# Performance work log

Measured on AMD Instinct MI355X. Metric: run time of the kernel, lower is better.

Reference implementation:

```python
import jax, jax.numpy as jnp
import numpy as np

B, T, D, H, V = 4096, 30, 512, 1024, 128  # words, MAX_WORD_LEN, input_dim, hidden, num_of_chars

def setup_inputs() -> dict:
    key = jax.random.key(0)
    ks = jax.random.split(key, 8)
    x = jax.random.randint(ks[0], (B, T), 0, V)
    emb = jax.random.normal(ks[1], (V, D), jnp.float32)
    s = 1.0 / np.sqrt(H)  # torch LSTMCell default init range
    W_ih = jax.random.uniform(ks[2], (4 * H, D), jnp.float32, -s, s)
    W_hh = jax.random.uniform(ks[3], (4 * H, H), jnp.float32, -s, s)
    b_ih = jax.random.uniform(ks[4], (4 * H,), jnp.float32, -s, s)
    b_hh = jax.random.uniform(ks[5], (4 * H,), jnp.float32, -s, s)
    xav = np.sqrt(2.0 / (B + H))  # xavier_normal_ std for [B,H] state tensors
    h0 = jax.random.normal(ks[6], (B, H), jnp.float32) * xav
    c0 = jax.random.normal(ks[7], (B, H), jnp.float32) * xav
    return {"x": x, "emb": emb, "W_ih": W_ih, "W_hh": W_hh,
            "b_ih": b_ih, "b_hh": b_hh, "h0": h0, "c0": c0}

def reference(x, emb, W_ih, W_hh, b_ih, b_hh, h0, c0):
    xe = emb[x]                       # [B, T, D] char embeddings
    xs = jnp.swapaxes(xe, 0, 1)       # [T, B, D] for scan over time

    def step(carry, xt):
        h, c = carry
        # torch LSTMCell gate order: i, f, g, o
        gates = xt @ W_ih.T + b_ih + h @ W_hh.T + b_hh  # [B, 4H]
        i, f, g, o = jnp.split(gates, 4, axis=-1)
        c = jax.nn.sigmoid(f) * c + jax.nn.sigmoid(i) * jnp.tanh(g)
        h = jax.nn.sigmoid(o) * jnp.tanh(c)
        return (h, c), None

    (h, c), _ = jax.lax.scan(step, (h0, c0), xs)
    return h
```

## Files before the change

kernel.cpp:

```cpp
#include <hip/hip_runtime.h>
#include <hip/hip_bf16.h>

#define BW    4096
#define TT    30
#define DIN   512
#define HD    1024
#define VCH   128
#define G4    4096

typedef __attribute__((ext_vector_type(8))) __bf16 bf16x8;
typedef __attribute__((ext_vector_type(4))) float  f32x4;

__device__ __forceinline__ ushort f2bf(float f) {
    unsigned u = __float_as_uint(f);
    unsigned r = (u + 0x7fffu + ((u >> 16) & 1u)) >> 16;
    return (ushort)r;
}
__device__ __forceinline__ float sigf(float x) { return 1.f / (1.f + __expf(-x)); }
__device__ __forceinline__ float tanhfast(float x) { return 2.f / (1.f + __expf(-2.f * x)) - 1.f; }


__global__ __launch_bounds__(256) void cvt_bf16_kernel(const float* __restrict__ in,
                                                       ushort* __restrict__ out, int n4) {
    int i = blockIdx.x * 256 + threadIdx.x;
    if (i >= n4) return;
    float4 v = ((const float4*)in)[i];
    ushort4 o;
    o.x = f2bf(v.x); o.y = f2bf(v.y); o.z = f2bf(v.z); o.w = f2bf(v.w);
    ((ushort4*)out)[i] = o;
}

__global__ __launch_bounds__(256) void init_hc_kernel(const float* __restrict__ h0,
                                                      const float* __restrict__ c0,
                                                      ushort* __restrict__ hb,
                                                      float* __restrict__ c, int n4) {
    int i = blockIdx.x * 256 + threadIdx.x;
    if (i >= n4) return;
    float4 v = ((const float4*)h0)[i];
    ushort4 o;
    o.x = f2bf(v.x); o.y = f2bf(v.y); o.z = f2bf(v.z); o.w = f2bf(v.w);
    ((ushort4*)hb)[i] = o;
    ((float4*)c)[i] = ((const float4*)c0)[i];
}

__global__ __launch_bounds__(256) void proj_emb_kernel(const float* __restrict__ emb,
                                                       const float* __restrict__ W_ih,
                                                       const float* __restrict__ b_ih,
                                                       const float* __restrict__ b_hh,
                                                       float* __restrict__ pe) {
    __shared__ float se[8][DIN];
    const int j  = blockIdx.x * 256 + threadIdx.x;
    const int c0 = blockIdx.y * 8;
    for (int i = threadIdx.x; i < 8 * DIN; i += 256)
        se[i >> 9][i & (DIN - 1)] = emb[(size_t)c0 * DIN + i];
    __syncthreads();
    const float* wv = W_ih + (size_t)j * DIN;
    float s[8];
#pragma unroll
    for (int cc = 0; cc < 8; ++cc) s[cc] = 0.f;
    for (int k = 0; k < DIN; k += 4) {
        float4 w4 = *(const float4*)&wv[k];
#pragma unroll
        for (int cc = 0; cc < 8; ++cc)
            s[cc] += se[cc][k] * w4.x + se[cc][k+1] * w4.y + se[cc][k+2] * w4.z + se[cc][k+3] * w4.w;
    }
    const float bias = b_ih[j] + b_hh[j];
    const int g = j >> 10, h = j & 1023;
#pragma unroll
    for (int cc = 0; cc < 8; ++cc)
        pe[(((size_t)(c0 + cc) * HD + h) << 2) + g] = s[cc] + bias;
}


#define STAGE2(AB, SB, SH, SKT)                                                        \
  {                                                                                    \
    ushort* dst0 = &tiles[((((SB)*2 + (AB))*2 + (SH)) * 8192) + (w*2+0)*512];          \
    ushort* dst1 = dst0 + 512;                                                         \
    const ushort *s0, *s1;                                                             \
    if ((AB) == 0) {                                                                   \
      s0 = A + aOff0 + (size_t)(SH)*131072 + (size_t)(SKT)*64;                         \
      s1 = A + aOff1 + (size_t)(SH)*131072 + (size_t)(SKT)*64;                         \
    } else {                                                                           \
      s0 = Bt + bOff[SH][0] + (size_t)(SKT)*64;                                        \
      s1 = Bt + bOff[SH][1] + (size_t)(SKT)*64;                                        \
    }                                                                                  \
    __builtin_amdgcn_global_load_lds((const __attribute__((address_space(1))) void*)s0,\
        (__attribute__((address_space(3))) void*)dst0, 16, 0, 0);                      \
    __builtin_amdgcn_global_load_lds((const __attribute__((address_space(1))) void*)s1,\
        (__attribute__((address_space(3))) void*)dst1, 16, 0, 0);                      \
  }

#define PHASE(BUF, Q, AB, SB, SH, SKT, VM)                                             \
  {                                                                                    \
    const ushort* aT = &tiles[(((BUF)*2 + 0)*2 + haA) * 8192];                         \
    const ushort* bT = &tiles[(((BUF)*2 + 1)*2 + haB) * 8192];                         \
    if ((Q) == 0) {                                                                    \
      _Pragma("unroll")                                                                \
      for (int n = 0; n < 4; ++n) {                                                    \
        bfr[n][0] = *(const bf16x8*)(bT + hbOff + n*1024 + aoff0);                     \
        bfr[n][1] = *(const bf16x8*)(bT + hbOff + n*1024 + aoff1);                     \
      }                                                                                \
    }                                                                                  \
    bf16x8 a00 = *(const bf16x8*)(aT + (2*(Q)+0)*1024 + aoff0);                        \
    bf16x8 a01 = *(const bf16x8*)(aT + (2*(Q)+0)*1024 + aoff1);                        \
    bf16x8 a10 = *(const bf16x8*)(aT + (2*(Q)+1)*1024 + aoff0);                        \
    bf16x8 a11 = *(const bf16x8*)(aT + (2*(Q)+1)*1024 + aoff1);                        \
    STAGE2(AB, SB, SH, SKT);                                                           \
    __builtin_amdgcn_s_barrier();                                                      \
    asm volatile("s_waitcnt lgkmcnt(0)" ::: "memory");                                 \
    __builtin_amdgcn_s_setprio(1);                                                     \
    _Pragma("unroll")                                                                  \
    for (int n = 0; n < 4; ++n) {                                                      \
      acc[2*(Q)+0][n] = __builtin_amdgcn_mfma_f32_16x16x32_bf16(a00, bfr[n][0], acc[2*(Q)+0][n], 0, 0, 0); \
      acc[2*(Q)+0][n] = __builtin_amdgcn_mfma_f32_16x16x32_bf16(a01, bfr[n][1], acc[2*(Q)+0][n], 0, 0, 0); \
      acc[2*(Q)+1][n] = __builtin_amdgcn_mfma_f32_16x16x32_bf16(a10, bfr[n][0], acc[2*(Q)+1][n], 0, 0, 0); \
      acc[2*(Q)+1][n] = __builtin_amdgcn_mfma_f32_16x16x32_bf16(a11, bfr[n][1], acc[2*(Q)+1][n], 0, 0, 0); \
    }                                                                                  \
    __builtin_amdgcn_s_setprio(0);                                                     \
    if (VM) asm volatile("s_waitcnt vmcnt(4)" ::: "memory");                           \
    __builtin_amdgcn_s_barrier();                                                      \
    asm volatile("" ::: "memory");                                                     \
  }

__global__ __launch_bounds__(512, 2) void gemm_cell_kernel(const ushort* __restrict__ A,
                                                           const ushort* __restrict__ Bt,
                                                           const float* __restrict__ peAll,
                                                           const int* __restrict__ x,
                                                           int t, int last,
                                                           float* __restrict__ c,
                                                           ushort* __restrict__ hbN,
                                                           float* __restrict__ hout) {
    __shared__ ushort tiles[65536];

    const int orig = blockIdx.x;
    const int wgid = (orig & 7) * 32 + (orig >> 3);
    const int bm = wgid >> 4, bn = wgid & 15;

    const int tid = threadIdx.x;
    const int w = tid >> 6, l = tid & 63;
    const int fr = l & 15, hi = l >> 4;
    const int haA = w >> 2;
    const int haB = (w >> 1) & 1;
    const int hbOff = (w & 1) * 4096;

    const int r0 = (w * 2 + 0) * 8 + (l >> 3), r1 = r0 + 8;
    const int csrc = (l & 7) ^ (l >> 3);
    const size_t aOff0 = (size_t)(bm * 256 + r0) * 1024 + csrc * 8;
    const size_t aOff1 = (size_t)(bm * 256 + r1) * 1024 + csrc * 8;
    size_t bOff[2][2];
#pragma unroll
    for (int half = 0; half < 2; ++half) {
        const int ra = half * 128 + r0, rb = half * 128 + r1;
        const int na = ((ra >> 4) & 3) * 1024 + bn * 64 + ((ra >> 6) << 4) + (ra & 15);
        const int nb = ((rb >> 4) & 3) * 1024 + bn * 64 + ((rb >> 6) << 4) + (rb & 15);
        bOff[half][0] = (size_t)na * 1024 + csrc * 8;
        bOff[half][1] = (size_t)nb * 1024 + csrc * 8;
    }

    const int aoff0 = fr * 64 + ((hi) ^ (fr & 7)) * 8;
    const int aoff1 = fr * 64 + ((4 + hi) ^ (fr & 7)) * 8;

    f32x4 acc[8][4];
#pragma unroll
    for (int m = 0; m < 8; ++m)
#pragma unroll
        for (int n = 0; n < 4; ++n) acc[m][n] = 0.f;
    bf16x8 bfr[4][2];

    STAGE2(0, 0, 0, 0);
    STAGE2(0, 0, 1, 0);
    STAGE2(1, 0, 0, 0);
    STAGE2(1, 0, 1, 0);
    STAGE2(1, 1, 0, 1);
    STAGE2(1, 1, 1, 1);
    asm volatile("s_waitcnt vmcnt(4)" ::: "memory");
    __builtin_amdgcn_s_barrier();
    asm volatile("" ::: "memory");

    for (int i = 0; i < 8; ++i) {
        const int k0 = 2 * i;
        PHASE(0, 0, 0, 1, 0, k0 + 1, 0);
        PHASE(0, 1, 0, 1, 1, k0 + 1, 0);
        PHASE(0, 2, 1, 0, 0, (k0 + 2) & 15, 0);
        PHASE(0, 3, 1, 0, 1, (k0 + 2) & 15, 1);
        PHASE(1, 0, 0, 0, 0, (k0 + 2) & 15, 0);
        PHASE(1, 1, 0, 0, 1, (k0 + 2) & 15, 0);
        PHASE(1, 2, 1, 1, 0, (k0 + 3) & 15, 0);
        PHASE(1, 3, 1, 1, 1, (k0 + 3) & 15, 1);
    }

    const int h_idx = bn * 64 + (w & 3) * 16 + fr;
    const int bbase = bm * 256 + (w >> 2) * 128 + (hi << 2);
    const float4* pe4 = (const float4*)peAll;
#pragma unroll
    for (int m = 0; m < 8; ++m) {
#pragma unroll
        for (int r = 0; r < 4; ++r) {
            const int b = bbase + m * 16 + r;
            const int ch = x[b * TT + t];
            const float4 pv = pe4[(size_t)ch * HD + h_idx];
            float I = sigf(acc[m][0][r] + pv.x);
            float F = sigf(acc[m][1][r] + pv.y);
            float G = tanhfast(acc[m][2][r] + pv.z);
            float O = sigf(acc[m][3][r] + pv.w);
            const size_t off = (size_t)b * HD + h_idx;
            const float cn = F * c[off] + I * G;
            const float hn = O * tanhfast(cn);
            c[off] = cn;
            hbN[off] = f2bf(hn);
            if (last) hout[off] = hn;
        }
    }
}

extern "C" void kernel_launch(void* const* d_in, const int* in_sizes, int n_in,
                              void* d_out, int out_size, void* d_ws, size_t ws_size,
                              hipStream_t stream) {
    const int*   x    = (const int*)d_in[0];
    const float* emb  = (const float*)d_in[1];
    const float* W_ih = (const float*)d_in[2];
    const float* W_hh = (const float*)d_in[3];
    const float* b_ih = (const float*)d_in[4];
    const float* b_hh = (const float*)d_in[5];
    const float* h0   = (const float*)d_in[6];
    const float* c0   = (const float*)d_in[7];
    float* out = (float*)d_out;

    char* ws = (char*)d_ws;
    ushort* whh = (ushort*)ws;
    float*  pe  = (float*)(ws + (size_t)8388608);
    ushort* hb0 = (ushort*)(ws + (size_t)(8388608 + 2097152));
    ushort* hb1 = (ushort*)(ws + (size_t)(8388608 + 2097152 + 8388608));
    float*  cbuf = (float*)(ws + (size_t)(8388608 + 2097152 + 8388608 + 8388608));

    cvt_bf16_kernel<<<4096, 256, 0, stream>>>(W_hh, whh, (G4 * HD) / 4);
    proj_emb_kernel<<<dim3(16, 16), 256, 0, stream>>>(emb, W_ih, b_ih, b_hh, pe);
    init_hc_kernel<<<4096, 256, 0, stream>>>(h0, c0, hb0, cbuf, (BW * HD) / 4);

    ushort* hbuf[2] = {hb0, hb1};
    for (int t = 0; t < TT; ++t) {
        gemm_cell_kernel<<<256, 512, 0, stream>>>(
            hbuf[t & 1], whh, pe, x, t, (t == TT - 1) ? 1 : 0,
            cbuf, hbuf[(t & 1) ^ 1], out);
    }
}
```

Baseline: 1.628 ms.

## Triple-buffer A tiles in LDS to deepen the GEMM prefetch pipeline

Grows the LDS tile buffer from 128KB to 160KB so that A tiles rotate through three buffers while B keeps two. Global-to-LDS loads for the next K-step can then be issued further ahead, and the vmcnt wait threshold rises from 4 to 8, letting more loads stay in flight behind the MFMA work. The cost is more LDS per block, which may limit blocks per CU, plus runtime-rotated buffer offsets in place of compile-time constants.

```diff
diff --git a/kernel.cpp b/kernel.cpp
--- a/kernel.cpp
+++ b/kernel.cpp
@@ -72,54 +72,54 @@
 }
 
 
-#define STAGE2(AB, SB, SH, SKT)                                                        \
-  {                                                                                    \
-    ushort* dst0 = &tiles[((((SB)*2 + (AB))*2 + (SH)) * 8192) + (w*2+0)*512];          \
-    ushort* dst1 = dst0 + 512;                                                         \
-    const ushort *s0, *s1;                                                             \
-    if ((AB) == 0) {                                                                   \
-      s0 = A + aOff0 + (size_t)(SH)*131072 + (size_t)(SKT)*64;                         \
-      s1 = A + aOff1 + (size_t)(SH)*131072 + (size_t)(SKT)*64;                         \
-    } else {                                                                           \
-      s0 = Bt + bOff[SH][0] + (size_t)(SKT)*64;                                        \
-      s1 = Bt + bOff[SH][1] + (size_t)(SKT)*64;                                        \
-    }                                                                                  \
-    __builtin_amdgcn_global_load_lds((const __attribute__((address_space(1))) void*)s0,\
-        (__attribute__((address_space(3))) void*)dst0, 16, 0, 0);                      \
-    __builtin_amdgcn_global_load_lds((const __attribute__((address_space(1))) void*)s1,\
-        (__attribute__((address_space(3))) void*)dst1, 16, 0, 0);                      \
+#define GLDS(SRC, DST)                                                                  \
+    __builtin_amdgcn_global_load_lds((const __attribute__((address_space(1))) void*)(SRC), \
+        (__attribute__((address_space(3))) void*)(DST), 16, 0, 0)
+
+#define STAGE_A(DSTOFF, SH, KOFF)                                                       \
+  {                                                                                     \
+    ushort* dst0 = &tiles[(DSTOFF) + (SH) * 8192 + w * 1024];                           \
+    GLDS(A + aOff0 + (size_t)(SH) * 131072 + (KOFF), dst0);                             \
+    GLDS(A + aOff1 + (size_t)(SH) * 131072 + (KOFF), dst0 + 512);                       \
   }
 
-#define PHASE(BUF, Q, AB, SB, SH, SKT, VM)                                             \
-  {                                                                                    \
-    const ushort* aT = &tiles[(((BUF)*2 + 0)*2 + haA) * 8192];                         \
-    const ushort* bT = &tiles[(((BUF)*2 + 1)*2 + haB) * 8192];                         \
-    if ((Q) == 0) {                                                                    \
-      _Pragma("unroll")                                                                \
-      for (int n = 0; n < 4; ++n) {                                                    \
-        bfr[n][0] = *(const bf16x8*)(bT + hbOff + n*1024 + aoff0);                     \
-        bfr[n][1] = *(const bf16x8*)(bT + hbOff + n*1024 + aoff1);                     \
-      }                                                                                \
-    }                                                                                  \
-    bf16x8 a00 = *(const bf16x8*)(aT + (2*(Q)+0)*1024 + aoff0);                        \
-    bf16x8 a01 = *(const bf16x8*)(aT + (2*(Q)+0)*1024 + aoff1);                        \
-    bf16x8 a10 = *(const bf16x8*)(aT + (2*(Q)+1)*1024 + aoff0);                        \
-    bf16x8 a11 = *(const bf16x8*)(aT + (2*(Q)+1)*1024 + aoff1);                        \
-    STAGE2(AB, SB, SH, SKT);                                                           \
-    __builtin_amdgcn_s_barrier();                                                      \
-    asm volatile("s_waitcnt lgkmcnt(0)" ::: "memory");                                 \
-    __builtin_amdgcn_s_setprio(1);                                                     \
-    _Pragma("unroll")                                                                  \
-    for (int n = 0; n < 4; ++n) {                                                      \
+#define STAGE_B(BIDX, SH, KOFF)                                                         \
+  {                                                                                     \
+    ushort* dst0 = &tiles[49152 + (BIDX) * 16384 + (SH) * 8192 + w * 1024];             \
+    GLDS(Bt + bOff[SH][0] + (KOFF), dst0);                                              \
+    GLDS(Bt + bOff[SH][1] + (KOFF), dst0 + 512);                                        \
+  }
+
+#define PHASE(ABASE, BIDX, Q, STAGE_STMT, VM)                                           \
+  {                                                                                     \
+    const ushort* aT = &tiles[(ABASE) + haA * 8192];                                    \
+    const ushort* bT = &tiles[49152 + (BIDX) * 16384 + haB * 8192];                     \
+    if ((Q) == 0) {                                                                     \
+      _Pragma("unroll")                                                                 \
+      for (int n = 0; n < 4; ++n) {                                                     \
+        bfr[n][0] = *(const bf16x8*)(bT + hbOff + n * 1024 + aoff0);                    \
+        bfr[n][1] = *(const bf16x8*)(bT + hbOff + n * 1024 + aoff1);                    \
+      }                                                                                 \
+    }                                                                                   \
+    bf16x8 a00 = *(const bf16x8*)(aT + (2 * (Q) + 0) * 1024 + aoff0);                   \
+    bf16x8 a01 = *(const bf16x8*)(aT + (2 * (Q) + 0) * 1024 + aoff1);                   \
+    bf16x8 a10 = *(const bf16x8*)(aT + (2 * (Q) + 1) * 1024 + aoff0);                   \
+    bf16x8 a11 = *(const bf16x8*)(aT + (2 * (Q) + 1) * 1024 + aoff1);                   \
+    STAGE_STMT;                                                                         \
+    __builtin_amdgcn_s_barrier();                                                       \
+    asm volatile("s_waitcnt lgkmcnt(0)" ::: "memory");                                  \
+    __builtin_amdgcn_s_setprio(1);                                                      \
+    _Pragma("unroll")                                                                   \
+    for (int n = 0; n < 4; ++n) {                                                       \
       acc[2*(Q)+0][n] = __builtin_amdgcn_mfma_f32_16x16x32_bf16(a00, bfr[n][0], acc[2*(Q)+0][n], 0, 0, 0); \
       acc[2*(Q)+0][n] = __builtin_amdgcn_mfma_f32_16x16x32_bf16(a01, bfr[n][1], acc[2*(Q)+0][n], 0, 0, 0); \
       acc[2*(Q)+1][n] = __builtin_amdgcn_mfma_f32_16x16x32_bf16(a10, bfr[n][0], acc[2*(Q)+1][n], 0, 0, 0); \
       acc[2*(Q)+1][n] = __builtin_amdgcn_mfma_f32_16x16x32_bf16(a11, bfr[n][1], acc[2*(Q)+1][n], 0, 0, 0); \
-    }                                                                                  \
-    __builtin_amdgcn_s_setprio(0);                                                     \
-    if (VM) asm volatile("s_waitcnt vmcnt(4)" ::: "memory");                           \
-    __builtin_amdgcn_s_barrier();                                                      \
-    asm volatile("" ::: "memory");                                                     \
+    }                                                                                   \
+    __builtin_amdgcn_s_setprio(0);                                                      \
+    if (VM) asm volatile("s_waitcnt vmcnt(8)" ::: "memory");                            \
+    __builtin_amdgcn_s_barrier();                                                       \
+    asm volatile("" ::: "memory");                                                      \
   }
 
 __global__ __launch_bounds__(512, 2) void gemm_cell_kernel(const ushort* __restrict__ A,
@@ -130,7 +130,7 @@
                                                            float* __restrict__ c,
                                                            ushort* __restrict__ hbN,
                                                            float* __restrict__ hout) {
-    __shared__ ushort tiles[65536];
+    __shared__ ushort tiles[81920];
 
     const int orig = blockIdx.x;
     const int wgid = (orig & 7) * 32 + (orig >> 3);
@@ -143,7 +143,7 @@
     const int haB = (w >> 1) & 1;
     const int hbOff = (w & 1) * 4096;
 
-    const int r0 = (w * 2 + 0) * 8 + (l >> 3), r1 = r0 + 8;
+    const int r0 = w * 16 + (l >> 3), r1 = r0 + 8;
     const int csrc = (l & 7) ^ (l >> 3);
     const size_t aOff0 = (size_t)(bm * 256 + r0) * 1024 + csrc * 8;
     const size_t aOff1 = (size_t)(bm * 256 + r1) * 1024 + csrc * 8;
@@ -167,27 +167,29 @@
         for (int n = 0; n < 4; ++n) acc[m][n] = 0.f;
     bf16x8 bfr[4][2];
 
-    STAGE2(0, 0, 0, 0);
-    STAGE2(0, 0, 1, 0);
-    STAGE2(1, 0, 0, 0);
-    STAGE2(1, 0, 1, 0);
-    STAGE2(1, 1, 0, 1);
-    STAGE2(1, 1, 1, 1);
-    asm volatile("s_waitcnt vmcnt(4)" ::: "memory");
+    STAGE_A(0, 0, 0);      STAGE_A(0, 1, 0);
+    STAGE_B(0, 0, 0);      STAGE_B(0, 1, 0);
+    STAGE_A(16384, 0, 64); STAGE_A(16384, 1, 64);
+    STAGE_B(1, 0, 64);     STAGE_B(1, 1, 64);
+    asm volatile("s_waitcnt vmcnt(8)" ::: "memory");
     __builtin_amdgcn_s_barrier();
     asm volatile("" ::: "memory");
 
+    unsigned rdA0 = 0, rdA1 = 16384, stA = 32768;
     for (int i = 0; i < 8; ++i) {
-        const int k0 = 2 * i;
-        PHASE(0, 0, 0, 1, 0, k0 + 1, 0);
-        PHASE(0, 1, 0, 1, 1, k0 + 1, 0);
-        PHASE(0, 2, 1, 0, 0, (k0 + 2) & 15, 0);
-        PHASE(0, 3, 1, 0, 1, (k0 + 2) & 15, 1);
-        PHASE(1, 0, 0, 0, 0, (k0 + 2) & 15, 0);
-        PHASE(1, 1, 0, 0, 1, (k0 + 2) & 15, 0);
-        PHASE(1, 2, 1, 1, 0, (k0 + 3) & 15, 0);
-        PHASE(1, 3, 1, 1, 1, (k0 + 3) & 15, 1);
-    }
+        const int kO2 = ((2 * i + 2) & 15) * 64;
+        const int kO3 = ((2 * i + 3) & 15) * 64;
+        PHASE(rdA0, 0, 0, STAGE_A(stA, 0, kO2), 0);
+        PHASE(rdA0, 0, 1, STAGE_A(stA, 1, kO2), 0);
+        PHASE(rdA0, 0, 2, STAGE_B(0, 0, kO2), 0);
+        PHASE(rdA0, 0, 3, STAGE_B(0, 1, kO2), 1);
+        PHASE(rdA1, 1, 0, STAGE_A(rdA0, 0, kO3), 0);
+        PHASE(rdA1, 1, 1, STAGE_A(rdA0, 1, kO3), 0);
+        PHASE(rdA1, 1, 2, STAGE_B(1, 0, kO3), 0);
+        PHASE(rdA1, 1, 3, STAGE_B(1, 1, kO3), 1);
+        const unsigned tmp = rdA0; rdA0 = stA; stA = rdA1; rdA1 = tmp;
+    }
+    asm volatile("s_waitcnt vmcnt(0)" ::: "memory");
 
     const int h_idx = bn * 64 + (w & 3) * 16 + fr;
     const int bbase = bm * 256 + (w >> 2) * 128 + (hi << 2);
```

Result: no change. 1.631 ms (+0.2%).
